# Kernel optimization log

Measured on AMD Instinct MI355X. Metric: run time of the kernel, lower is better.

## Reference

```python
import jax, jax.numpy as jnp
import numpy as np

B, H, NH, K = 4096, 2048, 8, 4
DH = H // NH
EPS = 1e-6      # sLSTM normalizer eps
LN_EPS = 1e-6   # flax LayerNorm default eps


def setup_inputs() -> dict:
    key = jax.random.key(0)
    ks = jax.random.split(key, 24)
    d = {}
    d["inputs"] = jax.random.normal(ks[0], (B, H), jnp.float32)
    d["c"] = jax.random.normal(ks[1], (B, H), jnp.float32)
    d["n"] = jax.random.uniform(ks[2], (B, H), jnp.float32)
    d["m"] = jax.random.normal(ks[3], (B, H), jnp.float32)
    d["h"] = jax.random.normal(ks[4], (B, H), jnp.float32)
    d["conv_state"] = jax.random.normal(ks[5], (B, K, H), jnp.float32)
    d["conv_kernel"] = jax.random.normal(ks[6], (K, H), jnp.float32) * 0.1
    d["conv_bias"] = jax.random.normal(ks[7], (H,), jnp.float32) * 0.1
    scale = 1.0 / np.sqrt(DH)
    for name, k in zip(["Wi", "Wf", "Wz", "Wo", "Ri", "Rf", "Rz", "Ro"], ks[8:16]):
        d[name] = jax.random.normal(k, (NH, DH, DH), jnp.float32) * scale
    for name, k in zip(["i_bias", "f_bias", "z_bias", "o_bias"], ks[16:20]):
        d[name] = jax.random.normal(k, (H,), jnp.float32) * 0.1
    d["ln_scale"] = jax.random.uniform(ks[20], (H,), jnp.float32, 0.5, 1.5)
    return d


def _block_diag(x, W):
    # x: (B, H), W: (NH, DH, DH) -> (B, H); per-head dense block
    return jnp.einsum("bhd,hde->bhe", x.reshape(B, NH, DH), W).reshape(B, H)


def reference(inputs, c, n, m, h, conv_state, conv_kernel, conv_bias,
              Wi, Wf, Wz, Wo, Ri, Rf, Rz, Ro,
              i_bias, f_bias, z_bias, o_bias, ln_scale):
    # --- causal depthwise conv, single step ---
    window = jnp.concatenate([conv_state[:, 1:, :], inputs[:, None, :]], axis=1)  # (B,K,H)
    conv_x = jnp.einsum("bkh,kh->bh", window, conv_kernel) + conv_bias
    conv_act = jax.nn.silu(conv_x)
    new_conv_state = window

    # --- input block-diagonal gate projections ---
    i = _block_diag(conv_act, Wi)
    f = _block_diag(conv_act, Wf)
    z = _block_diag(inputs, Wz)
    o = _block_diag(inputs, Wo)

    # --- recurrent block-diagonal projections + biases ---
    i = i + _block_diag(h, Ri) + i_bias
    f = f + _block_diag(h, Rf) + f_bias
    z = z + _block_diag(h, Rz) + z_bias
    o = o + _block_diag(h, Ro) + o_bias

    # --- stabilized exponential gating ---
    o = jax.nn.sigmoid(o)
    log_f = -jax.nn.softplus(-f)
    m_new = jnp.where(jnp.all(n == 0.0), i, jnp.maximum(log_f + m, i))
    i_p = jnp.minimum(jnp.exp(i - m_new), 1.0)
    f_p = jnp.minimum(jnp.exp(log_f + m - m_new), 1.0)
    c_new = f_p * c + i_p * jnp.tanh(z)
    n_new = f_p * n + i_p
    h_tilde = c_new / jnp.maximum(n_new, EPS)
    h_new = o * h_tilde

    # --- multi-head layer norm (per head over DH, scale only) ---
    y = h_new.reshape(B, NH, DH)
    mu = jnp.mean(y, axis=-1, keepdims=True)
    var = jnp.mean(jnp.square(y - mu), axis=-1, keepdims=True)
    y_n = (y - mu) * jax.lax.rsqrt(var + LN_EPS) * ln_scale.reshape(NH, DH)
    out = y_n.reshape(B, H)

    return out, c_new, n_new, m_new, h_new, new_conv_state
```

## Files before the change

### kernel.cpp

```cpp
#include <hip/hip_runtime.h>


#define Bn   4096
#define Hn   2048
#define NHn  8
#define DHn  256
#define BMr  32

typedef float     fl4  __attribute__((ext_vector_type(4)));
typedef _Float16  hf4  __attribute__((ext_vector_type(4)));
typedef float     f32x4 __attribute__((ext_vector_type(4)));

__device__ __forceinline__ float sigmoidf_(float x){ return 1.0f/(1.0f + __expf(-x)); }

__global__ __launch_bounds__(256) void prep_weights(
    const float* __restrict__ Wi, const float* __restrict__ Wf,
    const float* __restrict__ Wz, const float* __restrict__ Wo,
    const float* __restrict__ Ri, const float* __restrict__ Rf,
    const float* __restrict__ Rz, const float* __restrict__ Ro,
    _Float16* __restrict__ ws)
{
    int gid = blockIdx.x * 256 + threadIdx.x;
    int l   = gid & 63;
    int fid = gid >> 6;
    int nt  = fid & 1;
    int wv  = (fid >> 1) & 7;
    int g   = (fid >> 4) & 3;
    int kk  = (fid >> 6) & 15;
    int src = (fid >> 10) & 1;
    int hd  = (fid >> 11) & 7;

    const float* M;
    switch (src*4 + g) {
        case 0: M = Wi; break; case 1: M = Wf; break;
        case 2: M = Wz; break; case 3: M = Wo; break;
        case 4: M = Ri; break; case 5: M = Rf; break;
        case 6: M = Rz; break; default: M = Ro; break;
    }
    int e = wv*32 + nt*16 + (l & 15);
    int d = kk*16 + (l >> 4)*4;
    const float* p = M + ((size_t)hd*DHn + d)*DHn + e;
    hf4 v;
    v[0] = (_Float16)p[0];
    v[1] = (_Float16)p[DHn];
    v[2] = (_Float16)p[2*DHn];
    v[3] = (_Float16)p[3*DHn];
    *(hf4*)(ws + (size_t)fid*256 + l*4) = v;
}

__global__ __launch_bounds__(512) void slstm_fused(
    const float* __restrict__ inp, const float* __restrict__ pC,
    const float* __restrict__ pN,  const float* __restrict__ pM,
    const float* __restrict__ pH,  const float* __restrict__ cs,
    const float* __restrict__ ck,  const float* __restrict__ cb,
    const float* __restrict__ ib_, const float* __restrict__ fb_,
    const float* __restrict__ zb_, const float* __restrict__ ob_,
    const float* __restrict__ lns, const _Float16* __restrict__ ws,
    float* __restrict__ out)
{
    __shared__ __align__(16) unsigned char smem[49152];
    _Float16* aC = (_Float16*)smem;
    _Float16* aI = (_Float16*)(smem + 16384);
    _Float16* aH = (_Float16*)(smem + 32768);
    float*  hbuf = (float*)smem;

    const int tid = threadIdx.x;
    const int w   = tid >> 6;
    const int l   = tid & 63;
    const int lg  = l >> 4;
    const int lp  = l & 15;
    const int hd  = blockIdx.x & 7;
    const int mt  = blockIdx.x >> 3;
    const int brow = mt * BMr;
    const int hc   = hd * DHn;

    const size_t BH = (size_t)Bn * Hn;
    float* outY = out;
    float* outC = out +     BH;
    float* outN = out + 2 * BH;
    float* outM = out + 3 * BH;
    float* outH = out + 4 * BH;
    float* outS = out + 5 * BH;

    {
        int c4 = l * 4;
        fl4 k0 = *(const fl4*)(ck + 0*Hn + hc + c4);
        fl4 k1 = *(const fl4*)(ck + 1*Hn + hc + c4);
        fl4 k2 = *(const fl4*)(ck + 2*Hn + hc + c4);
        fl4 k3 = *(const fl4*)(ck + 3*Hn + hc + c4);
        fl4 bb = *(const fl4*)(cb + hc + c4);
        #pragma unroll
        for (int q = 0; q < 4; ++q) {
            int row = q*8 + w;
            size_t gr = (size_t)(brow + row);
            fl4 vin = *(const fl4*)(inp + gr*Hn + hc + c4);
            fl4 c1  = *(const fl4*)(cs + (gr*4 + 1)*Hn + hc + c4);
            fl4 c2  = *(const fl4*)(cs + (gr*4 + 2)*Hn + hc + c4);
            fl4 c3  = *(const fl4*)(cs + (gr*4 + 3)*Hn + hc + c4);
            fl4 vh  = *(const fl4*)(pH + gr*Hn + hc + c4);
            fl4 cx  = c1*k0 + c2*k1 + c3*k2 + vin*k3 + bb;
            fl4 ca;
            #pragma unroll
            for (int j = 0; j < 4; ++j) ca[j] = cx[j] * sigmoidf_(cx[j]);
            *(fl4*)(outS + (gr*4 + 0)*Hn + hc + c4) = c1;
            *(fl4*)(outS + (gr*4 + 1)*Hn + hc + c4) = c2;
            *(fl4*)(outS + (gr*4 + 2)*Hn + hc + c4) = c3;
            *(fl4*)(outS + (gr*4 + 3)*Hn + hc + c4) = vin;
            int ad = row*512 + ((l*8) ^ ((row & 15) << 3));
            hf4 hca, hin, hhh;
            #pragma unroll
            for (int j = 0; j < 4; ++j) {
                hca[j] = (_Float16)ca[j];
                hin[j] = (_Float16)vin[j];
                hhh[j] = (_Float16)vh[j];
            }
            *(hf4*)((char*)aC + ad) = hca;
            *(hf4*)((char*)aI + ad) = hin;
            *(hf4*)((char*)aH + ad) = hhh;
        }
    }
    __syncthreads();

    f32x4 acc[4][2][2];
    #pragma unroll
    for (int g = 0; g < 4; ++g)
        #pragma unroll
        for (int a = 0; a < 2; ++a)
            #pragma unroll
            for (int b = 0; b < 2; ++b)
                acc[g][a][b] = (f32x4)0.0f;

    const hf4* wsv = (const hf4*)ws;
    #pragma unroll
    for (int src = 0; src < 2; ++src) {
        const char* A_if = (const char*)(src ? aH : aC);
        const char* A_zo = (const char*)(src ? aH : aI);
        #pragma unroll 2
        for (int kk = 0; kk < 16; ++kk) {
            hf4 aif[2], azo[2];
            #pragma unroll
            for (int mt2 = 0; mt2 < 2; ++mt2) {
                int m   = mt2*16 + lp;
                int off = m*512 + ((kk*32 + lg*8) ^ ((m & 15) << 3));
                aif[mt2] = *(const hf4*)(A_if + off);
                azo[mt2] = (src == 1) ? aif[mt2] : *(const hf4*)(A_zo + off);
            }
            int fb0 = (((hd*2 + src)*16 + kk)*4)*16 + w*2;
            hf4 bf[4][2];
            #pragma unroll
            for (int g = 0; g < 4; ++g)
                #pragma unroll
                for (int nt = 0; nt < 2; ++nt)
                    bf[g][nt] = wsv[(size_t)(fb0 + g*16 + nt)*64 + l];
            #pragma unroll
            for (int g = 0; g < 4; ++g) {
                const hf4 A0 = (g < 2) ? aif[0] : azo[0];
                const hf4 A1 = (g < 2) ? aif[1] : azo[1];
                acc[g][0][0] = __builtin_amdgcn_mfma_f32_16x16x16f16(A0, bf[g][0], acc[g][0][0], 0, 0, 0);
                acc[g][0][1] = __builtin_amdgcn_mfma_f32_16x16x16f16(A0, bf[g][1], acc[g][0][1], 0, 0, 0);
                acc[g][1][0] = __builtin_amdgcn_mfma_f32_16x16x16f16(A1, bf[g][0], acc[g][1][0], 0, 0, 0);
                acc[g][1][1] = __builtin_amdgcn_mfma_f32_16x16x16f16(A1, bf[g][1], acc[g][1][1], 0, 0, 0);
            }
        }
    }

    __syncthreads();

    float ib[2], fb[2], zb[2], ob[2];
    #pragma unroll
    for (int nt = 0; nt < 2; ++nt) {
        int ncol = hc + w*32 + nt*16 + lp;
        ib[nt] = ib_[ncol]; fb[nt] = fb_[ncol];
        zb[nt] = zb_[ncol]; ob[nt] = ob_[ncol];
    }
    #pragma unroll
    for (int mt2 = 0; mt2 < 2; ++mt2) {
        #pragma unroll
        for (int r = 0; r < 4; ++r) {
            int rloc = mt2*16 + lg*4 + r;
            size_t grow = (size_t)(brow + rloc);
            #pragma unroll
            for (int nt = 0; nt < 2; ++nt) {
                int col = hc + w*32 + nt*16 + lp;
                size_t ad = grow*Hn + col;
                float iv = acc[0][mt2][nt][r] + ib[nt];
                float fv = acc[1][mt2][nt][r] + fb[nt];
                float zv = acc[2][mt2][nt][r] + zb[nt];
                float ov = acc[3][mt2][nt][r] + ob[nt];
                float c_o = pC[ad], n_o = pN[ad], m_o = pM[ad];
                float os  = sigmoidf_(ov);
                float lf  = fminf(fv, 0.0f) - log1pf(__expf(-fabsf(fv)));
                float mn  = fmaxf(lf + m_o, iv);
                float ipv = fminf(__expf(iv - mn), 1.0f);
                float fpv = fminf(__expf(lf + m_o - mn), 1.0f);
                float cn  = fpv * c_o + ipv * tanhf(zv);
                float nn  = fpv * n_o + ipv;
                float hn  = os * (cn / fmaxf(nn, 1e-6f));
                outC[ad] = cn; outN[ad] = nn; outM[ad] = mn; outH[ad] = hn;
                hbuf[rloc*260 + (w*32 + nt*16 + lp)] = hn;
            }
        }
    }
    __syncthreads();

    float ls[4];
    #pragma unroll
    for (int t = 0; t < 4; ++t) ls[t] = lns[hc + l + 64*t];
    #pragma unroll
    for (int rr = 0; rr < 4; ++rr) {
        int mloc = w*4 + rr;
        float v[4], s = 0.0f, sq = 0.0f;
        #pragma unroll
        for (int t = 0; t < 4; ++t) {
            v[t] = hbuf[mloc*260 + l + 64*t];
            s += v[t]; sq += v[t]*v[t];
        }
        #pragma unroll
        for (int d = 32; d; d >>= 1) {
            s  += __shfl_xor(s, d);
            sq += __shfl_xor(sq, d);
        }
        float mu   = s * (1.0f/256.0f);
        float var  = fmaxf(sq * (1.0f/256.0f) - mu*mu, 0.0f);
        float rstd = rsqrtf(var + 1e-6f);
        size_t grow = (size_t)(brow + mloc);
        #pragma unroll
        for (int t = 0; t < 4; ++t)
            outY[grow*Hn + hc + l + 64*t] = (v[t] - mu) * rstd * ls[t];
    }
}

extern "C" void kernel_launch(void* const* d_in, const int* in_sizes, int n_in,
                              void* d_out, int out_size, void* d_ws, size_t ws_size,
                              hipStream_t stream) {
    const float* inp = (const float*)d_in[0];
    const float* c_  = (const float*)d_in[1];
    const float* n_  = (const float*)d_in[2];
    const float* m_  = (const float*)d_in[3];
    const float* h_  = (const float*)d_in[4];
    const float* cs  = (const float*)d_in[5];
    const float* ck  = (const float*)d_in[6];
    const float* cb  = (const float*)d_in[7];
    const float* Wi  = (const float*)d_in[8];
    const float* Wf  = (const float*)d_in[9];
    const float* Wz  = (const float*)d_in[10];
    const float* Wo  = (const float*)d_in[11];
    const float* Ri  = (const float*)d_in[12];
    const float* Rf  = (const float*)d_in[13];
    const float* Rz  = (const float*)d_in[14];
    const float* Ro  = (const float*)d_in[15];
    const float* ib  = (const float*)d_in[16];
    const float* fb  = (const float*)d_in[17];
    const float* zb  = (const float*)d_in[18];
    const float* ob  = (const float*)d_in[19];
    const float* lns = (const float*)d_in[20];

    _Float16* ws = (_Float16*)d_ws;
    float* outp  = (float*)d_out;

    prep_weights<<<4096, 256, 0, stream>>>(Wi, Wf, Wz, Wo, Ri, Rf, Rz, Ro, ws);
    slstm_fused<<<1024, 512, 0, stream>>>(inp, c_, n_, m_, h_, cs, ck, cb,
                                          ib, fb, zb, ob, lns, ws, outp);
}
```

Measured before the change: 600.7 us.

## Swap MFMA operands so weights are A, shrink row tile to 16, vectorize epilogue

Halves the batch-row tile to 16 and launches twice as many blocks. It swaps the MFMA operands so the weights become the A operand, which gives each lane contiguous output columns and allows fl4 vector loads and stores of c/n/m and all outputs. The input and h fragments are now read from global memory and converted inline rather than staged in LDS, and the layer norm reduction uses shuffles plus a small LDS partial-sum table instead of a full h buffer. Fast-math exp, log and tanh replace the library calls, at a small accuracy risk, and each block now reads the weights twice as often relative to the rows it computes.

```diff
diff --git a/kernel.cpp b/kernel.cpp
--- a/kernel.cpp
+++ b/kernel.cpp
@@ -3,15 +3,16 @@
 
 #define Bn   4096
 #define Hn   2048
-#define NHn  8
 #define DHn  256
-#define BMr  32
+#define BMr  16
 
 typedef float     fl4  __attribute__((ext_vector_type(4)));
 typedef _Float16  hf4  __attribute__((ext_vector_type(4)));
+typedef _Float16  hf8  __attribute__((ext_vector_type(8)));
 typedef float     f32x4 __attribute__((ext_vector_type(4)));
 
-__device__ __forceinline__ float sigmoidf_(float x){ return 1.0f/(1.0f + __expf(-x)); }
+__device__ __forceinline__ hf4 lo8(hf8 v){ return __builtin_shufflevector(v, v, 0,1,2,3); }
+__device__ __forceinline__ hf4 hi8(hf8 v){ return __builtin_shufflevector(v, v, 4,5,6,7); }
 
 __global__ __launch_bounds__(256) void prep_weights(
     const float* __restrict__ Wi, const float* __restrict__ Wf,
@@ -22,13 +23,12 @@
 {
     int gid = blockIdx.x * 256 + threadIdx.x;
     int l   = gid & 63;
-    int fid = gid >> 6;
-    int nt  = fid & 1;
-    int wv  = (fid >> 1) & 7;
-    int g   = (fid >> 4) & 3;
-    int kk  = (fid >> 6) & 15;
-    int src = (fid >> 10) & 1;
-    int hd  = (fid >> 11) & 7;
+    int p   = gid >> 6;
+    int w   = p & 7;
+    int g   = (p >> 3) & 3;
+    int kk  = (p >> 5) & 15;
+    int src = (p >> 9) & 1;
+    int hd  = (p >> 10) & 7;
 
     const float* M;
     switch (src*4 + g) {
@@ -37,15 +37,17 @@
         case 4: M = Ri; break; case 5: M = Rf; break;
         case 6: M = Rz; break; default: M = Ro; break;
     }
-    int e = wv*32 + nt*16 + (l & 15);
-    int d = kk*16 + (l >> 4)*4;
-    const float* p = M + ((size_t)hd*DHn + d)*DHn + e;
-    hf4 v;
-    v[0] = (_Float16)p[0];
-    v[1] = (_Float16)p[DHn];
-    v[2] = (_Float16)p[2*DHn];
-    v[3] = (_Float16)p[3*DHn];
-    *(hf4*)(ws + (size_t)fid*256 + l*4) = v;
+    int dr = kk*16 + (l >> 4)*4;
+    const float* base = M + ((size_t)hd*DHn + dr)*DHn;
+    hf8 v;
+    #pragma unroll
+    for (int oc2 = 0; oc2 < 2; ++oc2) {
+        int e = w*32 + oc2*16 + (l & 15);
+        #pragma unroll
+        for (int j = 0; j < 4; ++j)
+            v[oc2*4 + j] = (_Float16)base[j*DHn + e];
+    }
+    *(hf8*)(ws + (size_t)p*512 + l*8) = v;
 }
 
 __global__ __launch_bounds__(512) void slstm_fused(
@@ -58,11 +60,8 @@
     const float* __restrict__ lns, const _Float16* __restrict__ ws,
     float* __restrict__ out)
 {
-    __shared__ __align__(16) unsigned char smem[49152];
-    _Float16* aC = (_Float16*)smem;
-    _Float16* aI = (_Float16*)(smem + 16384);
-    _Float16* aH = (_Float16*)(smem + 32768);
-    float*  hbuf = (float*)smem;
+    __shared__ __align__(16) _Float16 aC[BMr*DHn];
+    __shared__ float pls[16][8][2];
 
     const int tid = threadIdx.x;
     const int w   = tid >> 6;
@@ -83,150 +82,151 @@
     float* outS = out + 5 * BH;
 
     {
-        int c4 = l * 4;
-        fl4 k0 = *(const fl4*)(ck + 0*Hn + hc + c4);
-        fl4 k1 = *(const fl4*)(ck + 1*Hn + hc + c4);
-        fl4 k2 = *(const fl4*)(ck + 2*Hn + hc + c4);
-        fl4 k3 = *(const fl4*)(ck + 3*Hn + hc + c4);
-        fl4 bb = *(const fl4*)(cb + hc + c4);
-        #pragma unroll
-        for (int q = 0; q < 4; ++q) {
-            int row = q*8 + w;
-            size_t gr = (size_t)(brow + row);
-            fl4 vin = *(const fl4*)(inp + gr*Hn + hc + c4);
-            fl4 c1  = *(const fl4*)(cs + (gr*4 + 1)*Hn + hc + c4);
-            fl4 c2  = *(const fl4*)(cs + (gr*4 + 2)*Hn + hc + c4);
-            fl4 c3  = *(const fl4*)(cs + (gr*4 + 3)*Hn + hc + c4);
-            fl4 vh  = *(const fl4*)(pH + gr*Hn + hc + c4);
-            fl4 cx  = c1*k0 + c2*k1 + c3*k2 + vin*k3 + bb;
-            fl4 ca;
-            #pragma unroll
-            for (int j = 0; j < 4; ++j) ca[j] = cx[j] * sigmoidf_(cx[j]);
-            *(fl4*)(outS + (gr*4 + 0)*Hn + hc + c4) = c1;
-            *(fl4*)(outS + (gr*4 + 1)*Hn + hc + c4) = c2;
-            *(fl4*)(outS + (gr*4 + 2)*Hn + hc + c4) = c3;
-            *(fl4*)(outS + (gr*4 + 3)*Hn + hc + c4) = vin;
-            int ad = row*512 + ((l*8) ^ ((row & 15) << 3));
-            hf4 hca, hin, hhh;
-            #pragma unroll
-            for (int j = 0; j < 4; ++j) {
-                hca[j] = (_Float16)ca[j];
-                hin[j] = (_Float16)vin[j];
-                hhh[j] = (_Float16)vh[j];
-            }
-            *(hf4*)((char*)aC + ad) = hca;
-            *(hf4*)((char*)aI + ad) = hin;
-            *(hf4*)((char*)aH + ad) = hhh;
+        int row = tid >> 5;
+        int cg  = tid & 31;
+        int c8  = cg * 8;
+        const float* kp = ck + hc + c8;
+        fl4 k0a = *(const fl4*)(kp + 0*Hn), k0b = *(const fl4*)(kp + 0*Hn + 4);
+        fl4 k1a = *(const fl4*)(kp + 1*Hn), k1b = *(const fl4*)(kp + 1*Hn + 4);
+        fl4 k2a = *(const fl4*)(kp + 2*Hn), k2b = *(const fl4*)(kp + 2*Hn + 4);
+        fl4 k3a = *(const fl4*)(kp + 3*Hn), k3b = *(const fl4*)(kp + 3*Hn + 4);
+        fl4 bba = *(const fl4*)(cb + hc + c8), bbb = *(const fl4*)(cb + hc + c8 + 4);
+
+        size_t gr = (size_t)(brow + row);
+        const float* ip = inp + gr*Hn + hc + c8;
+        fl4 ia = *(const fl4*)(ip), ib2 = *(const fl4*)(ip + 4);
+        const float* cp = cs + (gr*4)*Hn + hc + c8;
+        fl4 c1a = *(const fl4*)(cp + 1*Hn), c1b = *(const fl4*)(cp + 1*Hn + 4);
+        fl4 c2a = *(const fl4*)(cp + 2*Hn), c2b = *(const fl4*)(cp + 2*Hn + 4);
+        fl4 c3a = *(const fl4*)(cp + 3*Hn), c3b = *(const fl4*)(cp + 3*Hn + 4);
+
+        fl4 cxa = c1a*k0a + c2a*k1a + c3a*k2a + ia *k3a + bba;
+        fl4 cxb = c1b*k0b + c2b*k1b + c3b*k2b + ib2*k3b + bbb;
+
+        float* sp = outS + (gr*4)*Hn + hc + c8;
+        *(fl4*)(sp + 0*Hn) = c1a;  *(fl4*)(sp + 0*Hn + 4) = c1b;
+        *(fl4*)(sp + 1*Hn) = c2a;  *(fl4*)(sp + 1*Hn + 4) = c2b;
+        *(fl4*)(sp + 2*Hn) = c3a;  *(fl4*)(sp + 2*Hn + 4) = c3b;
+        *(fl4*)(sp + 3*Hn) = ia;   *(fl4*)(sp + 3*Hn + 4) = ib2;
+
+        hf8 ca;
+        #pragma unroll
+        for (int j = 0; j < 4; ++j) {
+            float xa = cxa[j], xb = cxb[j];
+            ca[j]   = (_Float16)(xa * __fdividef(1.0f, 1.0f + __expf(-xa)));
+            ca[4+j] = (_Float16)(xb * __fdividef(1.0f, 1.0f + __expf(-xb)));
         }
+        char* aCb = (char*)aC;
+        int o0 = (c8*2) ^ ((row & 7) << 3);
+        *(hf4*)(aCb + row*512 + o0)       = lo8(ca);
+        *(hf4*)(aCb + row*512 + (o0 ^ 8)) = hi8(ca);
     }
     __syncthreads();
 
-    f32x4 acc[4][2][2];
-    #pragma unroll
-    for (int g = 0; g < 4; ++g)
-        #pragma unroll
-        for (int a = 0; a < 2; ++a)
-            #pragma unroll
-            for (int b = 0; b < 2; ++b)
-                acc[g][a][b] = (f32x4)0.0f;
-
-    const hf4* wsv = (const hf4*)ws;
-    #pragma unroll
-    for (int src = 0; src < 2; ++src) {
-        const char* A_if = (const char*)(src ? aH : aC);
-        const char* A_zo = (const char*)(src ? aH : aI);
-        #pragma unroll 2
-        for (int kk = 0; kk < 16; ++kk) {
-            hf4 aif[2], azo[2];
-            #pragma unroll
-            for (int mt2 = 0; mt2 < 2; ++mt2) {
-                int m   = mt2*16 + lp;
-                int off = m*512 + ((kk*32 + lg*8) ^ ((m & 15) << 3));
-                aif[mt2] = *(const hf4*)(A_if + off);
-                azo[mt2] = (src == 1) ? aif[mt2] : *(const hf4*)(A_zo + off);
-            }
-            int fb0 = (((hd*2 + src)*16 + kk)*4)*16 + w*2;
-            hf4 bf[4][2];
-            #pragma unroll
-            for (int g = 0; g < 4; ++g)
-                #pragma unroll
-                for (int nt = 0; nt < 2; ++nt)
-                    bf[g][nt] = wsv[(size_t)(fb0 + g*16 + nt)*64 + l];
-            #pragma unroll
-            for (int g = 0; g < 4; ++g) {
-                const hf4 A0 = (g < 2) ? aif[0] : azo[0];
-                const hf4 A1 = (g < 2) ? aif[1] : azo[1];
-                acc[g][0][0] = __builtin_amdgcn_mfma_f32_16x16x16f16(A0, bf[g][0], acc[g][0][0], 0, 0, 0);
-                acc[g][0][1] = __builtin_amdgcn_mfma_f32_16x16x16f16(A0, bf[g][1], acc[g][0][1], 0, 0, 0);
-                acc[g][1][0] = __builtin_amdgcn_mfma_f32_16x16x16f16(A1, bf[g][0], acc[g][1][0], 0, 0, 0);
-                acc[g][1][1] = __builtin_amdgcn_mfma_f32_16x16x16f16(A1, bf[g][1], acc[g][1][1], 0, 0, 0);
-            }
+    const size_t rB = (size_t)(brow + lp);
+    const int ob0 = hc + w*32 + lg*4;
+    fl4 cv[2], nv[2], mv[2];
+    #pragma unroll
+    for (int oc2 = 0; oc2 < 2; ++oc2) {
+        size_t ad = rB*Hn + ob0 + oc2*16;
+        cv[oc2] = *(const fl4*)(pC + ad);
+        nv[oc2] = *(const fl4*)(pN + ad);
+        mv[oc2] = *(const fl4*)(pM + ad);
+    }
+
+    f32x4 acc[4][2];
+    #pragma unroll
+    for (int g = 0; g < 4; ++g) { acc[g][0] = (f32x4)0.0f; acc[g][1] = (f32x4)0.0f; }
+
+    const hf8* wsv = (const hf8*)ws;
+    const int pb = ((hd*2)*16)*4*8 + w;
+    const char* aCb = (const char*)aC;
+    const float* inpF = inp + rB*Hn + hc;
+    const float* hF   = pH  + rB*Hn + hc;
+
+    #pragma unroll 4
+    for (int kk = 0; kk < 16; ++kk) {
+        int off = (kk*32 + lg*8) ^ ((lp & 7) << 3);
+        hf4 bCA = *(const hf4*)(aCb + lp*512 + off);
+        fl4 fi = *(const fl4*)(inpF + kk*16 + lg*4);
+        fl4 fh = *(const fl4*)(hF   + kk*16 + lg*4);
+        hf4 bIN, bH;
+        #pragma unroll
+        for (int j = 0; j < 4; ++j) { bIN[j] = (_Float16)fi[j]; bH[j] = (_Float16)fh[j]; }
+
+        #pragma unroll
+        for (int g = 0; g < 4; ++g) {
+            hf8 w0 = wsv[(size_t)(pb +       kk*32 + g*8)*64 + l];
+            hf8 w1 = wsv[(size_t)(pb + 512 + kk*32 + g*8)*64 + l];
+            hf4 x0 = (g < 2) ? bCA : bIN;
+            acc[g][0] = __builtin_amdgcn_mfma_f32_16x16x16f16(lo8(w0), x0, acc[g][0], 0, 0, 0);
+            acc[g][1] = __builtin_amdgcn_mfma_f32_16x16x16f16(hi8(w0), x0, acc[g][1], 0, 0, 0);
+            acc[g][0] = __builtin_amdgcn_mfma_f32_16x16x16f16(lo8(w1), bH, acc[g][0], 0, 0, 0);
+            acc[g][1] = __builtin_amdgcn_mfma_f32_16x16x16f16(hi8(w1), bH, acc[g][1], 0, 0, 0);
         }
     }
 
+    fl4 hv[2];
+    #pragma unroll
+    for (int oc2 = 0; oc2 < 2; ++oc2) {
+        int ob = ob0 + oc2*16;
+        fl4 ibv = *(const fl4*)(ib_ + ob);
+        fl4 fbv = *(const fl4*)(fb_ + ob);
+        fl4 zbv = *(const fl4*)(zb_ + ob);
+        fl4 obv = *(const fl4*)(ob_ + ob);
+        fl4 cno, nno, mno, hno;
+        #pragma unroll
+        for (int r = 0; r < 4; ++r) {
+            float iv = acc[0][oc2][r] + ibv[r];
+            float fv = acc[1][oc2][r] + fbv[r];
+            float zv = acc[2][oc2][r] + zbv[r];
+            float ov = acc[3][oc2][r] + obv[r];
+            float os = __fdividef(1.0f, 1.0f + __expf(-ov));
+            float lf = fminf(fv, 0.0f) - __logf(1.0f + __expf(-fabsf(fv)));
+            float mo = mv[oc2][r];
+            float mn2 = fmaxf(lf + mo, iv);
+            float ipv = fminf(__expf(iv - mn2), 1.0f);
+            float fpv = fminf(__expf(lf + mo - mn2), 1.0f);
+            float t  = __expf(-2.0f*fabsf(zv));
+            float tz = copysignf(__fdividef(1.0f - t, 1.0f + t), zv);
+            float cnv = fpv*cv[oc2][r] + ipv*tz;
+            float nnv = fpv*nv[oc2][r] + ipv;
+            float hnv = os * __fdividef(cnv, fmaxf(nnv, 1e-6f));
+            cno[r] = cnv; nno[r] = nnv; mno[r] = mn2; hno[r] = hnv;
+        }
+        size_t ad = rB*Hn + ob;
+        *(fl4*)(outC + ad) = cno;
+        *(fl4*)(outN + ad) = nno;
+        *(fl4*)(outM + ad) = mno;
+        *(fl4*)(outH + ad) = hno;
+        hv[oc2] = hno;
+    }
+
+    float s = 0.0f, sq = 0.0f;
+    #pragma unroll
+    for (int oc2 = 0; oc2 < 2; ++oc2)
+        #pragma unroll
+        for (int r = 0; r < 4; ++r) { float v = hv[oc2][r]; s += v; sq += v*v; }
+    s += __shfl_xor(s, 16); sq += __shfl_xor(sq, 16);
+    s += __shfl_xor(s, 32); sq += __shfl_xor(sq, 32);
+    if (lg == 0) { pls[lp][w][0] = s; pls[lp][w][1] = sq; }
     __syncthreads();
 
-    float ib[2], fb[2], zb[2], ob[2];
-    #pragma unroll
-    for (int nt = 0; nt < 2; ++nt) {
-        int ncol = hc + w*32 + nt*16 + lp;
-        ib[nt] = ib_[ncol]; fb[nt] = fb_[ncol];
-        zb[nt] = zb_[ncol]; ob[nt] = ob_[ncol];
-    }
-    #pragma unroll
-    for (int mt2 = 0; mt2 < 2; ++mt2) {
-        #pragma unroll
-        for (int r = 0; r < 4; ++r) {
-            int rloc = mt2*16 + lg*4 + r;
-            size_t grow = (size_t)(brow + rloc);
-            #pragma unroll
-            for (int nt = 0; nt < 2; ++nt) {
-                int col = hc + w*32 + nt*16 + lp;
-                size_t ad = grow*Hn + col;
-                float iv = acc[0][mt2][nt][r] + ib[nt];
-                float fv = acc[1][mt2][nt][r] + fb[nt];
-                float zv = acc[2][mt2][nt][r] + zb[nt];
-                float ov = acc[3][mt2][nt][r] + ob[nt];
-                float c_o = pC[ad], n_o = pN[ad], m_o = pM[ad];
-                float os  = sigmoidf_(ov);
-                float lf  = fminf(fv, 0.0f) - log1pf(__expf(-fabsf(fv)));
-                float mn  = fmaxf(lf + m_o, iv);
-                float ipv = fminf(__expf(iv - mn), 1.0f);
-                float fpv = fminf(__expf(lf + m_o - mn), 1.0f);
-                float cn  = fpv * c_o + ipv * tanhf(zv);
-                float nn  = fpv * n_o + ipv;
-                float hn  = os * (cn / fmaxf(nn, 1e-6f));
-                outC[ad] = cn; outN[ad] = nn; outM[ad] = mn; outH[ad] = hn;
-                hbuf[rloc*260 + (w*32 + nt*16 + lp)] = hn;
-            }
-        }
-    }
-    __syncthreads();
-
-    float ls[4];
-    #pragma unroll
-    for (int t = 0; t < 4; ++t) ls[t] = lns[hc + l + 64*t];
-    #pragma unroll
-    for (int rr = 0; rr < 4; ++rr) {
-        int mloc = w*4 + rr;
-        float v[4], s = 0.0f, sq = 0.0f;
-        #pragma unroll
-        for (int t = 0; t < 4; ++t) {
-            v[t] = hbuf[mloc*260 + l + 64*t];
-            s += v[t]; sq += v[t]*v[t];
-        }
-        #pragma unroll
-        for (int d = 32; d; d >>= 1) {
-            s  += __shfl_xor(s, d);
-            sq += __shfl_xor(sq, d);
-        }
-        float mu   = s * (1.0f/256.0f);
-        float var  = fmaxf(sq * (1.0f/256.0f) - mu*mu, 0.0f);
-        float rstd = rsqrtf(var + 1e-6f);
-        size_t grow = (size_t)(brow + mloc);
-        #pragma unroll
-        for (int t = 0; t < 4; ++t)
-            outY[grow*Hn + hc + l + 64*t] = (v[t] - mu) * rstd * ls[t];
+    const fl4* pr = (const fl4*)&pls[lp][0][0];
+    fl4 p0 = pr[0], p1 = pr[1], p2 = pr[2], p3 = pr[3];
+    float st  = p0[0] + p0[2] + p1[0] + p1[2] + p2[0] + p2[2] + p3[0] + p3[2];
+    float sqt = p0[1] + p0[3] + p1[1] + p1[3] + p2[1] + p2[3] + p3[1] + p3[3];
+    float mu   = st * (1.0f/256.0f);
+    float var  = fmaxf(sqt * (1.0f/256.0f) - mu*mu, 0.0f);
+    float rstd = rsqrtf(var + 1e-6f);
+    #pragma unroll
+    for (int oc2 = 0; oc2 < 2; ++oc2) {
+        int ob = ob0 + oc2*16;
+        fl4 ls = *(const fl4*)(lns + ob);
+        fl4 yo;
+        #pragma unroll
+        for (int r = 0; r < 4; ++r) yo[r] = (hv[oc2][r] - mu) * rstd * ls[r];
+        *(fl4*)(outY + rB*Hn + ob) = yo;
     }
 }
 
@@ -258,7 +258,7 @@
     _Float16* ws = (_Float16*)d_ws;
     float* outp  = (float*)d_out;
 
-    prep_weights<<<4096, 256, 0, stream>>>(Wi, Wf, Wz, Wo, Ri, Rf, Rz, Ro, ws);
-    slstm_fused<<<1024, 512, 0, stream>>>(inp, c_, n_, m_, h_, cs, ck, cb,
+    prep_weights<<<2048, 256, 0, stream>>>(Wi, Wf, Wz, Wo, Ri, Rf, Rz, Ro, ws);
+    slstm_fused<<<2048, 512, 0, stream>>>(inp, c_, n_, m_, h_, cs, ck, cb,
                                           ib, fb, zb, ob, lns, ws, outp);
 }
```

Measured after the change: 715.4 us. +19.1%, slower.
